# Kernel optimization log

Hardware: AMD Instinct MI355X
Metric: run time of the kernel (lower is better)

The kernel has to match this reference:

```python
import jax, jax.numpy as jnp
import numpy as np


def setup_inputs() -> dict:
    key = jax.random.key(0)
    ks = jax.random.split(key, 10)
    N, E, IN, H, OUT = 100000, 1250000, 64, 128, 64
    inp = {
        "x": jax.random.normal(ks[0], (N, IN), dtype=jnp.float32),
        "edge_index": jax.random.randint(ks[1], (2, E), 0, N, dtype=jnp.int64),
        "W1x": jax.random.normal(ks[2], (IN, H), dtype=jnp.float32) * 0.1,
        "b1x": jnp.zeros((H,), jnp.float32),
        "W2x": jax.random.normal(ks[3], (H, H), dtype=jnp.float32) * 0.1,
        "b2x": jnp.zeros((H,), jnp.float32),
        "W1a": jax.random.normal(ks[4], (IN, H), dtype=jnp.float32) * 0.1,
        "b1a": jnp.zeros((H,), jnp.float32),
        "W2a": jax.random.normal(ks[5], (H, H), dtype=jnp.float32) * 0.1,
        "b2a": jnp.zeros((H,), jnp.float32),
        "Wc": jax.random.normal(ks[6], (2 * H, H), dtype=jnp.float32) * 0.1,
        "bc": jnp.zeros((H,), jnp.float32),
        "Wcls": jax.random.normal(ks[7], (H, OUT), dtype=jnp.float32) * 0.1,
        "bcls": jnp.zeros((OUT,), jnp.float32),
        "num_nodes": N,
    }
    return inp


def _normalize_adj(edge_index, num_nodes):
    # add self loops, then D^{-1/2} A D^{-1/2} edge weights (deg counted on rows)
    loops = jnp.arange(num_nodes, dtype=edge_index.dtype)
    ei = jnp.concatenate([edge_index, jnp.stack([loops, loops])], axis=1)
    row, col = ei[0], ei[1]
    deg = jax.ops.segment_sum(jnp.ones(row.shape[0], jnp.float32), row,
                              num_segments=num_nodes)
    dinv = jnp.where(deg > 0, jax.lax.rsqrt(deg), 0.0)
    ew = dinv[row] * dinv[col]
    return row, col, ew


def reference(x, edge_index, W1x, b1x, W2x, b2x, W1a, b1a, W2a, b2a,
              Wc, bc, Wcls, bcls, num_nodes):
    row, col, ew = _normalize_adj(edge_index, num_nodes)
    # sparse adjacency aggregation: gather, scale, scatter-add
    agg = jax.ops.segment_sum(x[col] * ew[:, None], row, num_segments=num_nodes)
    # dual-branch MLPs
    h_x = jax.nn.relu(x @ W1x + b1x) @ W2x + b2x
    h_a = jax.nn.relu(agg @ W1a + b1a) @ W2a + b2a
    h = jnp.concatenate([h_x, h_a], axis=1) @ Wc + bc
    h = jax.nn.relu(h)  # dropout: eval mode (identity)
    return h @ Wcls + bcls
```

## Files before the change

### kernel.cpp

```cpp
#include <hip/hip_runtime.h>
#include <stdint.h>

typedef unsigned short u16;
typedef unsigned char u8;
typedef unsigned int u32;
typedef __attribute__((ext_vector_type(8))) short frag_ab;
typedef __attribute__((ext_vector_type(4))) float f32x4;

__device__ __forceinline__ u16 f2b(float f) {
  unsigned u = __float_as_uint(f);
  return (u16)((u + 0x7fffu + ((u >> 16) & 1u)) >> 16);
}
__device__ __forceinline__ float b2f(u16 u) {
  return __uint_as_float(((unsigned)u) << 16);
}

__device__ __forceinline__ int detect64(const int* __restrict__ ei32) {
  int v = ei32[2 * (threadIdx.x & 63) + 1];
  unsigned long long b = __ballot(v == 0);
  return (b == ~0ULL) ? 1 : 0;
}

__device__ __forceinline__ int edge_at(const void* ei, long pos, int is64) {
  if (is64) return (int)((const long long*)ei)[pos];
  return ((const int*)ei)[pos];
}

__global__ __launch_bounds__(256) void k_bhist_cvt(
    const void* __restrict__ ei, int E, int CH, int NB, int NBpad,
    int* __restrict__ bh,
    const float* __restrict__ x, u16* __restrict__ xb, u8* __restrict__ xq,
    long n64) {
  __shared__ int cnt[512];
  const int k = blockIdx.x, tid = threadIdx.x;
  const int is64 = detect64((const int*)ei);
  for (long i = ((long)k * 256 + tid) * 8; i < n64; i += 65536L * 8) {
    float4 v0 = *(const float4*)(x + i);
    float4 v1 = *(const float4*)(x + i + 4);
    frag_ab o;
    o[0] = (short)f2b(v0.x); o[1] = (short)f2b(v0.y);
    o[2] = (short)f2b(v0.z); o[3] = (short)f2b(v0.w);
    o[4] = (short)f2b(v1.x); o[5] = (short)f2b(v1.y);
    o[6] = (short)f2b(v1.z); o[7] = (short)f2b(v1.w);
    *(frag_ab*)(xb + i) = o;
    u32 p0 = (u32)__builtin_amdgcn_cvt_pk_fp8_f32(v0.x, v0.y, 0, false);
    p0 = (u32)__builtin_amdgcn_cvt_pk_fp8_f32(v0.z, v0.w, (int)p0, true);
    u32 p1 = (u32)__builtin_amdgcn_cvt_pk_fp8_f32(v1.x, v1.y, 0, false);
    p1 = (u32)__builtin_amdgcn_cvt_pk_fp8_f32(v1.z, v1.w, (int)p1, true);
    *(uint2*)(xq + i) = make_uint2(p0, p1);
  }
  for (int t = tid; t < NB; t += 256) cnt[t] = 0;
  __syncthreads();
  int e0 = k * CH, e1 = min(E, e0 + CH);
  for (int e = e0 + tid; e < e1; e += 256)
    atomicAdd(&cnt[edge_at(ei, e, is64) >> 9], 1);
  __syncthreads();
  for (int t = tid; t < NB; t += 256) bh[k * NBpad + t] = cnt[t];
}

__global__ __launch_bounds__(256) void k_cscan(
    int* __restrict__ bh, int* __restrict__ bstart, int NB, int NBpad, int E) {
  __shared__ int s[256];
  const int b = threadIdx.x;
  int tot = 0;
  if (b < NB)
    for (int k = 0; k < 256; ++k) tot += bh[k * NBpad + b];
  s[b] = (b < NB) ? tot : 0;
  __syncthreads();
  for (int off = 1; off < 256; off <<= 1) {
    int u = (b >= off) ? s[b - off] : 0;
    __syncthreads();
    s[b] += u;
    __syncthreads();
  }
  int excl = s[b] - tot;
  if (b < NB) {
    bstart[b] = excl;
    int run = excl;
    for (int k = 0; k < 256; ++k) {
      int t = bh[k * NBpad + b];
      bh[k * NBpad + b] = run;
      run += t;
    }
  }
  if (b == 0) bstart[NB] = E;
}

__global__ __launch_bounds__(256) void k_partition(
    const void* __restrict__ ei, int E, int CH, int NB, int NBpad,
    const int* __restrict__ bh, u32* __restrict__ staged) {
  __shared__ int cur[512];
  const int k = blockIdx.x, tid = threadIdx.x;
  const int is64 = detect64((const int*)ei);
  for (int t = tid; t < NB; t += 256) cur[t] = bh[k * NBpad + t];
  __syncthreads();
  int e0 = k * CH, e1 = min(E, e0 + CH);
  for (int e = e0 + tid; e < e1; e += 256) {
    int r = edge_at(ei, e, is64);
    int c = edge_at(ei, (long)E + e, is64);
    int pos = atomicAdd(&cur[r >> 9], 1);
    staged[pos] = ((u32)(r & 511) << 23) | (u32)c;
  }
}

__global__ __launch_bounds__(1024) void k_csr_bucket(
    const u32* __restrict__ staged, const int* __restrict__ bstart,
    int* __restrict__ rowptr, float* __restrict__ dinv,
    u32* __restrict__ cols, int N, int E) {
  __shared__ int cnt[512];
  __shared__ int cur[512];
  const int b = blockIdx.x, tid = threadIdx.x;
  const int r0 = b << 9;
  if (tid < 512) cnt[tid] = 0;
  __syncthreads();
  const int j0 = bstart[b], j1 = bstart[b + 1];
  for (int j = j0 + tid; j < j1; j += 1024)
    atomicAdd(&cnt[staged[j] >> 23], 1);
  __syncthreads();
  if (tid < 512) cur[tid] = cnt[tid];
  __syncthreads();
  for (int off = 1; off < 512; off <<= 1) {
    int v = 0;
    if (tid < 512 && tid >= off) v = cur[tid - off];
    __syncthreads();
    if (tid < 512) cur[tid] += v;
    __syncthreads();
  }
  int myStart = 0;
  if (tid < 512) {
    myStart = j0 + cur[tid] - cnt[tid];
    int r = r0 + tid;
    if (r < N) {
      rowptr[r] = myStart;
      dinv[r] = rsqrtf((float)cnt[tid] + 1.0f);
    }
  }
  __syncthreads();
  if (tid < 512) cur[tid] = myStart;
  if (b == 0 && tid == 0) rowptr[N] = E;
  __syncthreads();
  for (int j = j0 + tid; j < j1; j += 1024) {
    u32 v = staged[j];
    int rl = v >> 23;
    int pos = atomicAdd(&cur[rl], 1);
    cols[pos] = v & 0x7FFFFF;
  }
}

__global__ __launch_bounds__(256, 4) void k_aggregate(
    const int* __restrict__ rowptr, const u32* __restrict__ cols,
    const u16* __restrict__ xb, const u8* __restrict__ xq,
    const float* __restrict__ dinv, u16* __restrict__ aggb, int N) {
  int q = (blockIdx.x * 256 + threadIdx.x) >> 6;
  int f = threadIdx.x & 63;
  int r0 = q * 2, r1 = q * 2 + 1;
  if (r0 >= N) return;
  const bool has1 = (r1 < N);
  int j0 = rowptr[r0], e0 = rowptr[r0 + 1];
  int j1 = has1 ? rowptr[r1] : 0;
  int e1 = has1 ? rowptr[r1 + 1] : 0;
  float d0 = dinv[r0];
  float d1 = has1 ? dinv[r1] : 0.f;
  float acc0 = b2f(xb[(long)r0 * 64 + f]) * d0;
  float acc1 = has1 ? b2f(xb[(long)r1 * 64 + f]) * d1 : 0.f;
  while (j0 + 8 <= e0 && j1 + 8 <= e1) {
    int ca[8], cb[8];
#pragma unroll
    for (int i = 0; i < 8; ++i) { ca[i] = cols[j0 + i]; cb[i] = cols[j1 + i]; }
    int qa[8], qb[8];
    float wa[8], wb[8];
#pragma unroll
    for (int i = 0; i < 8; ++i) {
      qa[i] = xq[(long)ca[i] * 64 + f];
      qb[i] = xq[(long)cb[i] * 64 + f];
      wa[i] = dinv[ca[i]];
      wb[i] = dinv[cb[i]];
    }
    __builtin_amdgcn_sched_barrier(0);
#pragma unroll
    for (int i = 0; i < 8; ++i) {
      acc0 = fmaf(__builtin_amdgcn_cvt_f32_fp8(qa[i], 0), wa[i], acc0);
      acc1 = fmaf(__builtin_amdgcn_cvt_f32_fp8(qb[i], 0), wb[i], acc1);
    }
    j0 += 8; j1 += 8;
  }
  while (j0 + 4 <= e0 && j1 + 4 <= e1) {
    int ca[4], cb[4];
#pragma unroll
    for (int i = 0; i < 4; ++i) { ca[i] = cols[j0 + i]; cb[i] = cols[j1 + i]; }
    int qa[4], qb[4];
    float wa[4], wb[4];
#pragma unroll
    for (int i = 0; i < 4; ++i) {
      qa[i] = xq[(long)ca[i] * 64 + f];
      qb[i] = xq[(long)cb[i] * 64 + f];
      wa[i] = dinv[ca[i]];
      wb[i] = dinv[cb[i]];
    }
    __builtin_amdgcn_sched_barrier(0);
#pragma unroll
    for (int i = 0; i < 4; ++i) {
      acc0 = fmaf(__builtin_amdgcn_cvt_f32_fp8(qa[i], 0), wa[i], acc0);
      acc1 = fmaf(__builtin_amdgcn_cvt_f32_fp8(qb[i], 0), wb[i], acc1);
    }
    j0 += 4; j1 += 4;
  }
  for (; j0 + 4 <= e0; j0 += 4) {
    int c0 = cols[j0], c1 = cols[j0 + 1], c2 = cols[j0 + 2], c3 = cols[j0 + 3];
    int q0 = xq[(long)c0 * 64 + f];
    int q1 = xq[(long)c1 * 64 + f];
    int q2 = xq[(long)c2 * 64 + f];
    int q3 = xq[(long)c3 * 64 + f];
    acc0 = fmaf(__builtin_amdgcn_cvt_f32_fp8(q0, 0), dinv[c0], acc0);
    acc0 = fmaf(__builtin_amdgcn_cvt_f32_fp8(q1, 0), dinv[c1], acc0);
    acc0 = fmaf(__builtin_amdgcn_cvt_f32_fp8(q2, 0), dinv[c2], acc0);
    acc0 = fmaf(__builtin_amdgcn_cvt_f32_fp8(q3, 0), dinv[c3], acc0);
  }
  for (; j0 < e0; ++j0) {
    int c = cols[j0];
    acc0 = fmaf(__builtin_amdgcn_cvt_f32_fp8((int)xq[(long)c * 64 + f], 0),
                dinv[c], acc0);
  }
  for (; j1 + 4 <= e1; j1 += 4) {
    int c0 = cols[j1], c1 = cols[j1 + 1], c2 = cols[j1 + 2], c3 = cols[j1 + 3];
    int q0 = xq[(long)c0 * 64 + f];
    int q1 = xq[(long)c1 * 64 + f];
    int q2 = xq[(long)c2 * 64 + f];
    int q3 = xq[(long)c3 * 64 + f];
    acc1 = fmaf(__builtin_amdgcn_cvt_f32_fp8(q0, 0), dinv[c0], acc1);
    acc1 = fmaf(__builtin_amdgcn_cvt_f32_fp8(q1, 0), dinv[c1], acc1);
    acc1 = fmaf(__builtin_amdgcn_cvt_f32_fp8(q2, 0), dinv[c2], acc1);
    acc1 = fmaf(__builtin_amdgcn_cvt_f32_fp8(q3, 0), dinv[c3], acc1);
  }
  for (; j1 < e1; ++j1) {
    int c = cols[j1];
    acc1 = fmaf(__builtin_amdgcn_cvt_f32_fp8((int)xq[(long)c * 64 + f], 0),
                dinv[c], acc1);
  }
  aggb[(long)r0 * 64 + f] = f2b(acc0 * d0);
  if (has1) aggb[(long)r1 * 64 + f] = f2b(acc1 * d1);
}

__global__ __launch_bounds__(256) void k_wpack(
    const float* __restrict__ W1x, const float* __restrict__ W1a,
    const float* __restrict__ W2x, const float* __restrict__ W2a,
    const float* __restrict__ Wc, const float* __restrict__ b2x,
    const float* __restrict__ b2a, const float* __restrict__ bc,
    const float* __restrict__ Wcls,
    u16* __restrict__ W1xf, u16* __restrict__ W1af,
    u16* __restrict__ Wxpf, u16* __restrict__ Wapf,
    u16* __restrict__ Wclsf, float* __restrict__ bp) {
  const int blk = blockIdx.x, t = threadIdx.x;
  if (blk < 128) {
    const bool isX = blk < 64;
    int i = (isX ? blk : blk - 64) * 256 + t;
    const float* W2 = isX ? W2x : W2a;
    const float* wc = isX ? Wc : Wc + 128 * 128;
    int b = i & 7, l = (i >> 3) & 63, fi = i >> 9;
    int kb = fi & 3, nb = fi >> 2;
    int k = kb * 32 + (l >> 4) * 8 + b;
    int n = nb * 16 + (l & 15);
    float s = 0.f;
    for (int m = 0; m < 128; ++m) s = fmaf(W2[k * 128 + m], wc[m * 128 + n], s);
    (isX ? Wxpf : Wapf)[i] = f2b(s);
  } else if (blk < 224) {
    const float* W; u16* dst; int K, Nc, i0;
    if (blk < 160)      { W = W1x;  dst = W1xf;  K = 64;  Nc = 128; i0 = blk - 128; }
    else if (blk < 192) { W = W1a;  dst = W1af;  K = 64;  Nc = 128; i0 = blk - 160; }
    else                { W = Wcls; dst = Wclsf; K = 128; Nc = 64;  i0 = blk - 192; }
    int i = i0 * 256 + t;
    if (i < K * Nc) {
      int b = i & 7, l = (i >> 3) & 63, fi = i >> 9;
      int KB = K >> 5;
      int kb = fi % KB, nb = fi / KB;
      int k = kb * 32 + (l >> 4) * 8 + b;
      int n = nb * 16 + (l & 15);
      dst[i] = f2b(W[k * Nc + n]);
    }
  } else if (t < 128) {
    float s = bc[t];
    for (int m = 0; m < 128; ++m)
      s += b2x[m] * Wc[m * 128 + t] + b2a[m] * Wc[(128 + m) * 128 + t];
    bp[t] = s;
  }
}

__global__ __launch_bounds__(256, 2) void k_mlp(
    const u16* __restrict__ xb, const u16* __restrict__ aggb,
    const u16* __restrict__ W1xf, const u16* __restrict__ W1af,
    const float* __restrict__ b1x, const float* __restrict__ b1a,
    const u16* __restrict__ Wxpf, const u16* __restrict__ Wapf,
    const float* __restrict__ bp,
    const u16* __restrict__ Wclsf, const float* __restrict__ bcls,
    float* __restrict__ out, int N) {
  __shared__ u16 S[4][16 * 256];
  const int w = threadIdx.x >> 6;
  const int lane = threadIdx.x & 63;
  const int m0 = blockIdx.x * 64 + w * 16;
  const int lm = lane & 15;
  const int lq = lane >> 4;
  u16* s = S[w];

  for (int br = 0; br < 2; ++br) {
    const u16* A = br ? aggb : xb;
    const u16* Wf = br ? W1af : W1xf;
    const float* bias = br ? b1a : b1x;
    const u16* ap = A + (long)(m0 + lm) * 64 + lq * 8;
    frag_ab a0 = *(const frag_ab*)(ap);
    frag_ab a1 = *(const frag_ab*)(ap + 32);
    frag_ab B1[16];
#pragma unroll
    for (int i = 0; i < 16; ++i)
      B1[i] = *(const frag_ab*)(Wf + (size_t)(i * 64 + lane) * 8);
    __builtin_amdgcn_sched_barrier(0);
#pragma unroll
    for (int nb = 0; nb < 8; ++nb) {
      f32x4 acc = {0.f, 0.f, 0.f, 0.f};
      acc = __builtin_amdgcn_mfma_f32_16x16x32_bf16(a0, B1[nb * 2], acc, 0, 0, 0);
      acc = __builtin_amdgcn_mfma_f32_16x16x32_bf16(a1, B1[nb * 2 + 1], acc, 0, 0, 0);
      int col = nb * 16 + lm;
      float bv = bias[col];
#pragma unroll
      for (int r = 0; r < 4; ++r) {
        int row = lq * 4 + r;
        s[(row * 256 + br * 128 + col) ^ ((row & 7) << 3)] =
            f2b(fmaxf(acc[r] + bv, 0.f));
      }
    }
  }
  __builtin_amdgcn_wave_barrier();

  frag_ab hfr[8];
#pragma unroll
  for (int kb = 0; kb < 8; ++kb)
    hfr[kb] = *(const frag_ab*)&s[(lm * 256 + kb * 32 + lq * 8) ^ ((lm & 7) << 3)];
  __builtin_amdgcn_wave_barrier();
#pragma unroll
  for (int nbp = 0; nbp < 4; ++nbp) {
    frag_ab B2[16];
#pragma unroll
    for (int h = 0; h < 2; ++h) {
      int nb = nbp * 2 + h;
#pragma unroll
      for (int kb = 0; kb < 8; ++kb) {
        const u16* Wf2 = (kb < 4) ? Wxpf : Wapf;
        B2[h * 8 + kb] =
            *(const frag_ab*)(Wf2 + (size_t)((nb * 4 + (kb & 3)) * 64 + lane) * 8);
      }
    }
    __builtin_amdgcn_sched_barrier(0);
#pragma unroll
    for (int h = 0; h < 2; ++h) {
      int nb = nbp * 2 + h;
      f32x4 acc = {0.f, 0.f, 0.f, 0.f};
#pragma unroll
      for (int kb = 0; kb < 8; ++kb)
        acc = __builtin_amdgcn_mfma_f32_16x16x32_bf16(hfr[kb], B2[h * 8 + kb], acc, 0, 0, 0);
      int col = nb * 16 + lm;
      float bv = bp[col];
#pragma unroll
      for (int r = 0; r < 4; ++r) {
        int row = lq * 4 + r;
        s[(row * 128 + col) ^ ((row & 7) << 3)] = f2b(fmaxf(acc[r] + bv, 0.f));
      }
    }
  }
  __builtin_amdgcn_wave_barrier();

  frag_ab h3[4];
#pragma unroll
  for (int kb = 0; kb < 4; ++kb)
    h3[kb] = *(const frag_ab*)&s[(lm * 128 + kb * 32 + lq * 8) ^ ((lm & 7) << 3)];
  frag_ab B3[16];
#pragma unroll
  for (int i = 0; i < 16; ++i)
    B3[i] = *(const frag_ab*)(Wclsf + (size_t)(i * 64 + lane) * 8);
  __builtin_amdgcn_sched_barrier(0);
#pragma unroll
  for (int nb = 0; nb < 4; ++nb) {
    f32x4 acc = {0.f, 0.f, 0.f, 0.f};
#pragma unroll
    for (int kb = 0; kb < 4; ++kb)
      acc = __builtin_amdgcn_mfma_f32_16x16x32_bf16(h3[kb], B3[nb * 4 + kb], acc, 0, 0, 0);
    int col = nb * 16 + lm;
    float bv = bcls[col];
#pragma unroll
    for (int r = 0; r < 4; ++r) {
      int grow = m0 + lq * 4 + r;
      if (grow < N) out[(long)grow * 64 + col] = acc[r] + bv;
    }
  }
}

extern "C" void kernel_launch(void* const* d_in, const int* in_sizes, int n_in,
                              void* d_out, int out_size, void* d_ws, size_t ws_size,
                              hipStream_t stream) {
  const float* x    = (const float*)d_in[0];
  const void*  ei   = d_in[1];
  const float* W1x  = (const float*)d_in[2];
  const float* b1x  = (const float*)d_in[3];
  const float* W2x  = (const float*)d_in[4];
  const float* b2x  = (const float*)d_in[5];
  const float* W1a  = (const float*)d_in[6];
  const float* b1a  = (const float*)d_in[7];
  const float* W2a  = (const float*)d_in[8];
  const float* b2a  = (const float*)d_in[9];
  const float* Wc   = (const float*)d_in[10];
  const float* bc   = (const float*)d_in[11];
  const float* Wcls = (const float*)d_in[12];
  const float* bcls = (const float*)d_in[13];
  const int N = in_sizes[0] / 64;
  const int E = in_sizes[1] / 2;

  const int NB = (N + 511) >> 9;
  const int NBpad = (NB + 63) & ~63;
  const int CH = (E + 255) / 256;

  float* ws = (float*)d_ws;
  long nAlign = (N + 255) & ~255L;
  float* dinv = ws;
  int*   rowptr = (int*)(ws + nAlign);
  u16*   xb   = (u16*)(ws + 2 * nAlign + 256);
  u16*   aggb = xb + (long)N * 64;
  u8*    xq   = (u8*)(aggb + (long)N * 64);
  float* bp   = (float*)(xq + ((long)N * 64 + 255 & ~255L));
  u16*   W1xf = (u16*)(bp + 128);
  u16*   W1af = W1xf + 8192;
  u16*   Wxpf = W1af + 8192;
  u16*   Wapf = Wxpf + 16384;
  u16*   Wclsf = Wapf + 16384;
  int*   bh   = (int*)(Wclsf + 8192);
  int*   bstart = bh + 256 * NBpad;
  u32*   staged = (u32*)(bstart + NB + 64);
  u32*   cols   = staged + E;
  float* out = (float*)d_out;

  k_bhist_cvt<<<256, 256, 0, stream>>>(ei, E, CH, NB, NBpad, bh, x, xb, xq,
                                       (long)N * 64);
  k_cscan<<<1, 256, 0, stream>>>(bh, bstart, NB, NBpad, E);
  k_partition<<<256, 256, 0, stream>>>(ei, E, CH, NB, NBpad, bh, staged);
  k_csr_bucket<<<NB, 1024, 0, stream>>>(staged, bstart, rowptr, dinv, cols, N, E);
  k_aggregate<<<(N + 7) / 8, 256, 0, stream>>>(rowptr, cols, xb, xq, dinv, aggb, N);
  k_wpack<<<225, 256, 0, stream>>>(W1x, W1a, W2x, W2a, Wc, b2x, b2a, bc, Wcls,
                                   W1xf, W1af, Wxpf, Wapf, Wclsf, bp);
  k_mlp<<<(N + 63) / 64, 256, 0, stream>>>(xb, aggb, W1xf, W1af, b1x, b1a,
                                           Wxpf, Wapf, bp, Wclsf, bcls, out, N);
}
```

Measured before the change: 151.4 us.

## Stage MLP weight fragments through shared memory instead of per-wave global loads

Each block now cooperatively copies weight matrices (W1x/W1a, then Wxp, Wap, Wcls in phases) into a 32KB shared buffer, and waves read B fragments from LDS instead of each wave loading them from global memory into registers. The second layer is split into two K-halves with persistent accumulators so each half's weights fit in the buffer. This cuts redundant global/L2 weight traffic and register pressure, but adds several block-wide __syncthreads and more LDS use, which may reduce occupancy and serialize the phases.

Result: no change. 151.7 us (+0.2%).

```diff
diff --git a/kernel.cpp b/kernel.cpp
--- a/kernel.cpp
+++ b/kernel.cpp
@@ -294,30 +294,40 @@
     const u16* __restrict__ Wclsf, const float* __restrict__ bcls,
     float* __restrict__ out, int N) {
   __shared__ u16 S[4][16 * 256];
-  const int w = threadIdx.x >> 6;
-  const int lane = threadIdx.x & 63;
+  __shared__ u16 WS[16384];
+  const int tid = threadIdx.x;
+  const int w = tid >> 6;
+  const int lane = tid & 63;
   const int m0 = blockIdx.x * 64 + w * 16;
   const int lm = lane & 15;
   const int lq = lane >> 4;
   u16* s = S[w];
 
+  {
+    const uint4* s1 = (const uint4*)W1xf;
+    const uint4* s2 = (const uint4*)W1af;
+    uint4* d = (uint4*)WS;
+#pragma unroll
+    for (int i = 0; i < 4; ++i) d[tid + i * 256] = s1[tid + i * 256];
+#pragma unroll
+    for (int i = 0; i < 4; ++i) d[1024 + tid + i * 256] = s2[tid + i * 256];
+  }
+  __syncthreads();
+
   for (int br = 0; br < 2; ++br) {
     const u16* A = br ? aggb : xb;
-    const u16* Wf = br ? W1af : W1xf;
+    const u16* Wl = WS + (br ? 8192 : 0);
     const float* bias = br ? b1a : b1x;
     const u16* ap = A + (long)(m0 + lm) * 64 + lq * 8;
     frag_ab a0 = *(const frag_ab*)(ap);
     frag_ab a1 = *(const frag_ab*)(ap + 32);
-    frag_ab B1[16];
-#pragma unroll
-    for (int i = 0; i < 16; ++i)
-      B1[i] = *(const frag_ab*)(Wf + (size_t)(i * 64 + lane) * 8);
-    __builtin_amdgcn_sched_barrier(0);
 #pragma unroll
     for (int nb = 0; nb < 8; ++nb) {
+      frag_ab b0 = *(const frag_ab*)(Wl + (size_t)((nb * 2 + 0) * 64 + lane) * 8);
+      frag_ab b1v = *(const frag_ab*)(Wl + (size_t)((nb * 2 + 1) * 64 + lane) * 8);
       f32x4 acc = {0.f, 0.f, 0.f, 0.f};
-      acc = __builtin_amdgcn_mfma_f32_16x16x32_bf16(a0, B1[nb * 2], acc, 0, 0, 0);
-      acc = __builtin_amdgcn_mfma_f32_16x16x32_bf16(a1, B1[nb * 2 + 1], acc, 0, 0, 0);
+      acc = __builtin_amdgcn_mfma_f32_16x16x32_bf16(a0, b0, acc, 0, 0, 0);
+      acc = __builtin_amdgcn_mfma_f32_16x16x32_bf16(a1, b1v, acc, 0, 0, 0);
       int col = nb * 16 + lm;
       float bv = bias[col];
 #pragma unroll
@@ -328,60 +338,75 @@
       }
     }
   }
-  __builtin_amdgcn_wave_barrier();
 
   frag_ab hfr[8];
 #pragma unroll
   for (int kb = 0; kb < 8; ++kb)
     hfr[kb] = *(const frag_ab*)&s[(lm * 256 + kb * 32 + lq * 8) ^ ((lm & 7) << 3)];
-  __builtin_amdgcn_wave_barrier();
-#pragma unroll
-  for (int nbp = 0; nbp < 4; ++nbp) {
-    frag_ab B2[16];
-#pragma unroll
-    for (int h = 0; h < 2; ++h) {
-      int nb = nbp * 2 + h;
-#pragma unroll
-      for (int kb = 0; kb < 8; ++kb) {
-        const u16* Wf2 = (kb < 4) ? Wxpf : Wapf;
-        B2[h * 8 + kb] =
-            *(const frag_ab*)(Wf2 + (size_t)((nb * 4 + (kb & 3)) * 64 + lane) * 8);
-      }
-    }
-    __builtin_amdgcn_sched_barrier(0);
-#pragma unroll
-    for (int h = 0; h < 2; ++h) {
-      int nb = nbp * 2 + h;
-      f32x4 acc = {0.f, 0.f, 0.f, 0.f};
-#pragma unroll
-      for (int kb = 0; kb < 8; ++kb)
-        acc = __builtin_amdgcn_mfma_f32_16x16x32_bf16(hfr[kb], B2[h * 8 + kb], acc, 0, 0, 0);
-      int col = nb * 16 + lm;
-      float bv = bp[col];
-#pragma unroll
-      for (int r = 0; r < 4; ++r) {
-        int row = lq * 4 + r;
-        s[(row * 128 + col) ^ ((row & 7) << 3)] = f2b(fmaxf(acc[r] + bv, 0.f));
-      }
-    }
-  }
-  __builtin_amdgcn_wave_barrier();
+  __syncthreads();
+
+  {
+    const uint4* s1 = (const uint4*)Wxpf;
+    uint4* d = (uint4*)WS;
+#pragma unroll
+    for (int i = 0; i < 8; ++i) d[tid + i * 256] = s1[tid + i * 256];
+  }
+  __syncthreads();
+  f32x4 accs[8];
+#pragma unroll
+  for (int nb = 0; nb < 8; ++nb) accs[nb] = (f32x4){0.f, 0.f, 0.f, 0.f};
+#pragma unroll
+  for (int nb = 0; nb < 8; ++nb)
+#pragma unroll
+    for (int kb = 0; kb < 4; ++kb) {
+      frag_ab b = *(const frag_ab*)(WS + (size_t)((nb * 4 + kb) * 64 + lane) * 8);
+      accs[nb] = __builtin_amdgcn_mfma_f32_16x16x32_bf16(hfr[kb], b, accs[nb], 0, 0, 0);
+    }
+  __syncthreads();
+
+  {
+    const uint4* s1 = (const uint4*)Wapf;
+    uint4* d = (uint4*)WS;
+#pragma unroll
+    for (int i = 0; i < 8; ++i) d[tid + i * 256] = s1[tid + i * 256];
+  }
+  __syncthreads();
+#pragma unroll
+  for (int nb = 0; nb < 8; ++nb) {
+#pragma unroll
+    for (int kb = 0; kb < 4; ++kb) {
+      frag_ab b = *(const frag_ab*)(WS + (size_t)((nb * 4 + kb) * 64 + lane) * 8);
+      accs[nb] = __builtin_amdgcn_mfma_f32_16x16x32_bf16(hfr[4 + kb], b, accs[nb], 0, 0, 0);
+    }
+    int col = nb * 16 + lm;
+    float bv = bp[col];
+#pragma unroll
+    for (int r = 0; r < 4; ++r) {
+      int row = lq * 4 + r;
+      s[(row * 128 + col) ^ ((row & 7) << 3)] = f2b(fmaxf(accs[nb][r] + bv, 0.f));
+    }
+  }
 
   frag_ab h3[4];
 #pragma unroll
   for (int kb = 0; kb < 4; ++kb)
     h3[kb] = *(const frag_ab*)&s[(lm * 128 + kb * 32 + lq * 8) ^ ((lm & 7) << 3)];
-  frag_ab B3[16];
-#pragma unroll
-  for (int i = 0; i < 16; ++i)
-    B3[i] = *(const frag_ab*)(Wclsf + (size_t)(i * 64 + lane) * 8);
-  __builtin_amdgcn_sched_barrier(0);
+  __syncthreads();
+  {
+    const uint4* s1 = (const uint4*)Wclsf;
+    uint4* d = (uint4*)WS;
+#pragma unroll
+    for (int i = 0; i < 4; ++i) d[tid + i * 256] = s1[tid + i * 256];
+  }
+  __syncthreads();
 #pragma unroll
   for (int nb = 0; nb < 4; ++nb) {
     f32x4 acc = {0.f, 0.f, 0.f, 0.f};
 #pragma unroll
-    for (int kb = 0; kb < 4; ++kb)
-      acc = __builtin_amdgcn_mfma_f32_16x16x32_bf16(h3[kb], B3[nb * 4 + kb], acc, 0, 0, 0);
+    for (int kb = 0; kb < 4; ++kb) {
+      frag_ab b = *(const frag_ab*)(WS + (size_t)((nb * 4 + kb) * 64 + lane) * 8);
+      acc = __builtin_amdgcn_mfma_f32_16x16x32_bf16(h3[kb], b, acc, 0, 0, 0);
+    }
     int col = nb * 16 + lm;
     float bv = bcls[col];
 #pragma unroll
```

## Process two 16-row tiles per wave in MLP kernel to reuse weight fragments

Applied to the files above, without the earlier changes.

Each wave now computes 32 rows (two 16-row MFMA tiles) instead of 16, so every weight fragment loaded from global memory feeds two MFMAs. The per-wave LDS staging buffer doubles and the grid halves. Bulk weight prefetch with sched_barriers is replaced by inline per-nb loads, trading explicit latency hiding for fewer live registers and halved weight traffic. Higher LDS use per block may reduce occupancy.

Result: no change. 149.1 us (-1.5%).

```diff
diff --git a/kernel.cpp b/kernel.cpp
--- a/kernel.cpp
+++ b/kernel.cpp
@@ -293,10 +293,10 @@
     const float* __restrict__ bp,
     const u16* __restrict__ Wclsf, const float* __restrict__ bcls,
     float* __restrict__ out, int N) {
-  __shared__ u16 S[4][16 * 256];
+  __shared__ u16 S[4][32 * 256];
   const int w = threadIdx.x >> 6;
   const int lane = threadIdx.x & 63;
-  const int m0 = blockIdx.x * 64 + w * 16;
+  const int m0 = blockIdx.x * 128 + w * 32;
   const int lm = lane & 15;
   const int lq = lane >> 4;
   u16* s = S[w];
@@ -305,90 +305,96 @@
     const u16* A = br ? aggb : xb;
     const u16* Wf = br ? W1af : W1xf;
     const float* bias = br ? b1a : b1x;
-    const u16* ap = A + (long)(m0 + lm) * 64 + lq * 8;
-    frag_ab a0 = *(const frag_ab*)(ap);
-    frag_ab a1 = *(const frag_ab*)(ap + 32);
-    frag_ab B1[16];
-#pragma unroll
-    for (int i = 0; i < 16; ++i)
-      B1[i] = *(const frag_ab*)(Wf + (size_t)(i * 64 + lane) * 8);
-    __builtin_amdgcn_sched_barrier(0);
+    frag_ab a[2][2];
+#pragma unroll
+    for (int rt = 0; rt < 2; ++rt) {
+      const u16* ap = A + (long)(m0 + rt * 16 + lm) * 64 + lq * 8;
+      a[rt][0] = *(const frag_ab*)(ap);
+      a[rt][1] = *(const frag_ab*)(ap + 32);
+    }
 #pragma unroll
     for (int nb = 0; nb < 8; ++nb) {
-      f32x4 acc = {0.f, 0.f, 0.f, 0.f};
-      acc = __builtin_amdgcn_mfma_f32_16x16x32_bf16(a0, B1[nb * 2], acc, 0, 0, 0);
-      acc = __builtin_amdgcn_mfma_f32_16x16x32_bf16(a1, B1[nb * 2 + 1], acc, 0, 0, 0);
+      frag_ab b0 = *(const frag_ab*)(Wf + (size_t)((nb * 2 + 0) * 64 + lane) * 8);
+      frag_ab b1v = *(const frag_ab*)(Wf + (size_t)((nb * 2 + 1) * 64 + lane) * 8);
       int col = nb * 16 + lm;
       float bv = bias[col];
 #pragma unroll
+      for (int rt = 0; rt < 2; ++rt) {
+        f32x4 acc = {0.f, 0.f, 0.f, 0.f};
+        acc = __builtin_amdgcn_mfma_f32_16x16x32_bf16(a[rt][0], b0, acc, 0, 0, 0);
+        acc = __builtin_amdgcn_mfma_f32_16x16x32_bf16(a[rt][1], b1v, acc, 0, 0, 0);
+#pragma unroll
+        for (int r = 0; r < 4; ++r) {
+          int row = rt * 16 + lq * 4 + r;
+          s[(row * 256 + br * 128 + col) ^ ((row & 7) << 3)] =
+              f2b(fmaxf(acc[r] + bv, 0.f));
+        }
+      }
+    }
+  }
+  __builtin_amdgcn_wave_barrier();
+
+  frag_ab hfr[2][8];
+#pragma unroll
+  for (int rt = 0; rt < 2; ++rt)
+#pragma unroll
+    for (int kb = 0; kb < 8; ++kb) {
+      int row = rt * 16 + lm;
+      hfr[rt][kb] =
+          *(const frag_ab*)&s[(row * 256 + kb * 32 + lq * 8) ^ ((lm & 7) << 3)];
+    }
+  __builtin_amdgcn_wave_barrier();
+#pragma unroll
+  for (int nb = 0; nb < 8; ++nb) {
+    f32x4 acc[2] = {{0.f, 0.f, 0.f, 0.f}, {0.f, 0.f, 0.f, 0.f}};
+#pragma unroll
+    for (int kb = 0; kb < 8; ++kb) {
+      const u16* Wf2 = (kb < 4) ? Wxpf : Wapf;
+      frag_ab b = *(const frag_ab*)(Wf2 + (size_t)((nb * 4 + (kb & 3)) * 64 + lane) * 8);
+#pragma unroll
+      for (int rt = 0; rt < 2; ++rt)
+        acc[rt] = __builtin_amdgcn_mfma_f32_16x16x32_bf16(hfr[rt][kb], b, acc[rt], 0, 0, 0);
+    }
+    int col = nb * 16 + lm;
+    float bv = bp[col];
+#pragma unroll
+    for (int rt = 0; rt < 2; ++rt)
+#pragma unroll
       for (int r = 0; r < 4; ++r) {
-        int row = lq * 4 + r;
-        s[(row * 256 + br * 128 + col) ^ ((row & 7) << 3)] =
-            f2b(fmaxf(acc[r] + bv, 0.f));
+        int row = rt * 16 + lq * 4 + r;
+        s[(row * 128 + col) ^ ((row & 7) << 3)] = f2b(fmaxf(acc[rt][r] + bv, 0.f));
       }
-    }
   }
   __builtin_amdgcn_wave_barrier();
 
-  frag_ab hfr[8];
-#pragma unroll
-  for (int kb = 0; kb < 8; ++kb)
-    hfr[kb] = *(const frag_ab*)&s[(lm * 256 + kb * 32 + lq * 8) ^ ((lm & 7) << 3)];
-  __builtin_amdgcn_wave_barrier();
-#pragma unroll
-  for (int nbp = 0; nbp < 4; ++nbp) {
-    frag_ab B2[16];
-#pragma unroll
-    for (int h = 0; h < 2; ++h) {
-      int nb = nbp * 2 + h;
-#pragma unroll
-      for (int kb = 0; kb < 8; ++kb) {
-        const u16* Wf2 = (kb < 4) ? Wxpf : Wapf;
-        B2[h * 8 + kb] =
-            *(const frag_ab*)(Wf2 + (size_t)((nb * 4 + (kb & 3)) * 64 + lane) * 8);
-      }
-    }
-    __builtin_amdgcn_sched_barrier(0);
-#pragma unroll
-    for (int h = 0; h < 2; ++h) {
-      int nb = nbp * 2 + h;
-      f32x4 acc = {0.f, 0.f, 0.f, 0.f};
-#pragma unroll
-      for (int kb = 0; kb < 8; ++kb)
-        acc = __builtin_amdgcn_mfma_f32_16x16x32_bf16(hfr[kb], B2[h * 8 + kb], acc, 0, 0, 0);
-      int col = nb * 16 + lm;
-      float bv = bp[col];
-#pragma unroll
-      for (int r = 0; r < 4; ++r) {
-        int row = lq * 4 + r;
-        s[(row * 128 + col) ^ ((row & 7) << 3)] = f2b(fmaxf(acc[r] + bv, 0.f));
-      }
-    }
-  }
-  __builtin_amdgcn_wave_barrier();
-
-  frag_ab h3[4];
-#pragma unroll
-  for (int kb = 0; kb < 4; ++kb)
-    h3[kb] = *(const frag_ab*)&s[(lm * 128 + kb * 32 + lq * 8) ^ ((lm & 7) << 3)];
-  frag_ab B3[16];
-#pragma unroll
-  for (int i = 0; i < 16; ++i)
-    B3[i] = *(const frag_ab*)(Wclsf + (size_t)(i * 64 + lane) * 8);
-  __builtin_amdgcn_sched_barrier(0);
+  frag_ab h3[2][4];
+#pragma unroll
+  for (int rt = 0; rt < 2; ++rt)
+#pragma unroll
+    for (int kb = 0; kb < 4; ++kb) {
+      int row = rt * 16 + lm;
+      h3[rt][kb] =
+          *(const frag_ab*)&s[(row * 128 + kb * 32 + lq * 8) ^ ((lm & 7) << 3)];
+    }
 #pragma unroll
   for (int nb = 0; nb < 4; ++nb) {
-    f32x4 acc = {0.f, 0.f, 0.f, 0.f};
-#pragma unroll
-    for (int kb = 0; kb < 4; ++kb)
-      acc = __builtin_amdgcn_mfma_f32_16x16x32_bf16(h3[kb], B3[nb * 4 + kb], acc, 0, 0, 0);
+    f32x4 acc[2] = {{0.f, 0.f, 0.f, 0.f}, {0.f, 0.f, 0.f, 0.f}};
+#pragma unroll
+    for (int kb = 0; kb < 4; ++kb) {
+      frag_ab b = *(const frag_ab*)(Wclsf + (size_t)((nb * 4 + kb) * 64 + lane) * 8);
+#pragma unroll
+      for (int rt = 0; rt < 2; ++rt)
+        acc[rt] = __builtin_amdgcn_mfma_f32_16x16x32_bf16(h3[rt][kb], b, acc[rt], 0, 0, 0);
+    }
     int col = nb * 16 + lm;
     float bv = bcls[col];
 #pragma unroll
-    for (int r = 0; r < 4; ++r) {
-      int grow = m0 + lq * 4 + r;
-      if (grow < N) out[(long)grow * 64 + col] = acc[r] + bv;
-    }
+    for (int rt = 0; rt < 2; ++rt)
+#pragma unroll
+      for (int r = 0; r < 4; ++r) {
+        int grow = m0 + rt * 16 + lq * 4 + r;
+        if (grow < N) out[(long)grow * 64 + col] = acc[rt][r] + bv;
+      }
   }
 }
 
@@ -443,6 +449,6 @@
   k_aggregate<<<(N + 7) / 8, 256, 0, stream>>>(rowptr, cols, xb, xq, dinv, aggb, N);
   k_wpack<<<225, 256, 0, stream>>>(W1x, W1a, W2x, W2a, Wc, b2x, b2a, bc, Wcls,
                                    W1xf, W1af, Wxpf, Wapf, Wclsf, bp);
-  k_mlp<<<(N + 63) / 64, 256, 0, stream>>>(xb, aggb, W1xf, W1af, b1x, b1a,
-                                           Wxpf, Wapf, bp, Wclsf, bcls, out, N);
-}
+  k_mlp<<<(N + 127) / 128, 256, 0, stream>>>(xb, aggb, W1xf, W1af, b1x, b1a,
+                                             Wxpf, Wapf, bp, Wclsf, bcls, out, N);
+}
```
